# Kernel tuning notes

Hardware: AMD Instinct MI355X
Metric: run time of the kernel (lower is better)

Reference implementation:

```python
import jax, jax.numpy as jnp
import numpy as np

D_MODEL = 1024
SEQ_LEN = 2048
NUM_EIGH = 24
BATCH = 4


def _spectral_filters(L, K):
    # Hankel matrix Z[i,j] = 2 / ((i+j)^3 - (i+j)), 1-indexed; top-K eigvecs scaled by sigma^0.25
    t = np.arange(1, L + 1, dtype=np.float64)
    s = t[:, None] + t[None, :]
    Z = 2.0 / (s ** 3 - s)
    sigma, phi = np.linalg.eigh(Z)
    phi_k = phi[:, -K:] * (sigma[-K:] ** 0.25)
    return jnp.asarray(phi_k, dtype=jnp.float32)


def setup_inputs() -> dict:
    key = jax.random.key(0)
    k1, k2, k3 = jax.random.split(key, 3)
    std = 1.0 / np.sqrt(D_MODEL)
    return {
        "x": jax.random.normal(k1, (BATCH, SEQ_LEN, D_MODEL), dtype=jnp.float32),
        "M_inputs": jax.random.normal(k2, (D_MODEL, D_MODEL), dtype=jnp.float32) * std,
        "M_filters": jax.random.normal(k3, (NUM_EIGH, D_MODEL), dtype=jnp.float32) * std,
        "phi": _spectral_filters(SEQ_LEN, NUM_EIGH),
    }


def _convolve_approx(u, v, n):
    # u: [B, L, D] inputs (already projected); v: [L, D] per-channel causal filters.
    # Dual-branch causal FFT convolution:
    #   plus[b,t,d]  = sum_{s<=t} v[s,d] * u[b,t-s,d]
    #   minus[b,t,d] = (-1)^t * sum_{s<=t} v[s,d] * (-1)^{t-s} u[b,t-s,d]
    B, L, D = u.shape
    sgn = jnp.where(jnp.arange(L) % 2 == 0, 1.0, -1.0).astype(u.dtype)[None, :, None]  # [1,L,1]
    V = jnp.fft.rfft(v, n=n, axis=0)                     # [F, D] complex
    U = jnp.stack([u, u * sgn], axis=-1)                 # [B, L, D, 2]
    Uf = jnp.fft.rfft(U, n=n, axis=1)                    # [B, F, D, 2]
    conv = jnp.fft.irfft(V[None, :, :, None] * Uf, n=n, axis=1)[:, :L]  # [B, L, D, 2]
    return conv[..., 0], conv[..., 1] * sgn


def reference(x, M_inputs, M_filters, phi):
    L = x.shape[1]
    n = 1 << int(np.ceil(np.log2(2 * L - 1)))  # next pow2 of 2L-1 (static)
    x_proj = x @ M_inputs                       # [B, L, D]
    phi_proj = phi[:L] @ M_filters              # [L, D]
    spectral_plus, spectral_minus = _convolve_approx(x_proj, phi_proj, n)
    return spectral_plus + spectral_minus
```

## Files before the change

### kernel.cpp

```cpp
#include <hip/hip_runtime.h>
#include <stdint.h>

#define D_MODEL 1024
#define SEQ 2048
#define HALF 1024
#define K_EIG 24
#define GUARD4 24
#define K4 128
#define K4P (GUARD4 + K4)
#define WE_JP4 72

typedef __attribute__((ext_vector_type(8))) short bf16x8;
typedef __attribute__((ext_vector_type(4))) float f32x4;
typedef _Float16 f16;
typedef _Float16 f16x2 __attribute__((ext_vector_type(2)));
typedef unsigned int uint;

#define GAS __attribute__((address_space(1)))
#define LAS __attribute__((address_space(3)))

static __device__ __forceinline__ unsigned short f2bf(float f) {
  union { float f; uint32_t u; } v; v.f = f;
  uint32_t u = v.u;
  u += 0x7FFFu + ((u >> 16) & 1u);
  return (unsigned short)(u >> 16);
}

static __device__ __forceinline__ float dot2(uint w2, uint u2, float c) {
  return __builtin_amdgcn_fdot2(__builtin_bit_cast(f16x2, w2),
                                __builtin_bit_cast(f16x2, u2), c, false);
}

static __device__ __forceinline__ uint pkrtz(float lo, float hi) {
  return __builtin_bit_cast(uint, __builtin_amdgcn_cvt_pkrtz(lo, hi));
}

__global__ void k_convert_x(const float* __restrict__ x, unsigned short* __restrict__ xb, int n4) {
  int idx = blockIdx.x * blockDim.x + threadIdx.x;
  if (idx < n4) {
    float4 v = ((const float4*)x)[idx];
    ushort4 o;
    o.x = f2bf(v.x); o.y = f2bf(v.y); o.z = f2bf(v.z); o.w = f2bf(v.w);
    ((ushort4*)xb)[idx] = o;
  }
}

__global__ void k_zero_guard(uint4* __restrict__ u4) {
  int idx = blockIdx.x * 256 + threadIdx.x;
  int r = blockIdx.y;
  u4[(size_t)r * (K4P * 1024) + idx] = make_uint4(0u, 0u, 0u, 0u);
}

__global__ void k_transpose_M(const float* __restrict__ M, unsigned short* __restrict__ Mt) {
  __shared__ float tile[32][33];
  int k0 = blockIdx.y * 32, n0 = blockIdx.x * 32;
  int tx = threadIdx.x & 31, ty = threadIdx.x >> 5;
  #pragma unroll
  for (int r = 0; r < 32; r += 8)
    tile[ty + r][tx] = M[(size_t)(k0 + ty + r) * D_MODEL + n0 + tx];
  __syncthreads();
  #pragma unroll
  for (int r = 0; r < 32; r += 8)
    Mt[(size_t)(n0 + ty + r) * D_MODEL + k0 + tx] = f2bf(tile[tx][ty + r]);
}

__global__ __launch_bounds__(256) void k_we4(const float* __restrict__ phi,
                                             const float* __restrict__ Mf,
                                             uint4* __restrict__ we4) {
  const int jp4 = blockIdx.x;
  const int d = blockIdx.y * 256 + threadIdx.x;
  if (jp4 >= 64) {
    we4[(size_t)jp4 * D_MODEL + d] = make_uint4(0u, 0u, 0u, 0u);
    return;
  }
  __shared__ float ph[8][K_EIG];
  if (threadIdx.x < 8 * K_EIG) {
    int s = threadIdx.x / K_EIG, k = threadIdx.x - s * K_EIG;
    ph[s][k] = phi[(size_t)(16 * jp4 + 2 * s) * K_EIG + k];
  }
  __syncthreads();
  float s[8] = {};
  #pragma unroll
  for (int k = 0; k < K_EIG; ++k) {
    float mv = Mf[(size_t)k * D_MODEL + d];
    #pragma unroll
    for (int j = 0; j < 8; ++j) s[j] = fmaf(ph[j][k], mv, s[j]);
  }
  uint4 o;
  o.x = pkrtz(2.f * s[0], 2.f * s[1]);
  o.y = pkrtz(2.f * s[2], 2.f * s[3]);
  o.z = pkrtz(2.f * s[4], 2.f * s[5]);
  o.w = pkrtz(2.f * s[6], 2.f * s[7]);
  we4[(size_t)jp4 * D_MODEL + d] = o;
}

__global__ __launch_bounds__(256) void k_gemm(const unsigned short* __restrict__ A,
                                              const unsigned short* __restrict__ Bt,
                                              uint* __restrict__ Ug) {
  __shared__ unsigned short As[128 * 32];
  __shared__ unsigned short Bs[128 * 32];
  const int m0 = (int)blockIdx.x * 128;
  const int n0 = (int)blockIdx.y * 128;
  const int tid = threadIdx.x;
  const int lane = tid & 63;
  const int wave = tid >> 6;
  const int wm = wave >> 1, wn = wave & 1;
  const int srow = lane >> 2;
  const int skoff = (lane & 3) * 8;

  f32x4 acc[4][4] = {};

  for (int k0 = 0; k0 < 1024; k0 += 32) {
    __syncthreads();
    #pragma unroll
    for (int c = 0; c < 2; ++c) {
      int rbase = wave * 32 + c * 16;
      const unsigned short* src = A + (size_t)(m0 + rbase + srow) * 1024 + k0 + skoff;
      __builtin_amdgcn_global_load_lds((const GAS void*)src, (LAS void*)(As + rbase * 32), 16, 0, 0);
    }
    #pragma unroll
    for (int c = 0; c < 2; ++c) {
      int rbase = wave * 32 + c * 16;
      const unsigned short* src = Bt + (size_t)(n0 + rbase + srow) * 1024 + k0 + skoff;
      __builtin_amdgcn_global_load_lds((const GAS void*)src, (LAS void*)(Bs + rbase * 32), 16, 0, 0);
    }
    __syncthreads();

    bf16x8 a[4], b[4];
    #pragma unroll
    for (int mt = 0; mt < 4; ++mt)
      a[mt] = *(const bf16x8*)(As + ((wm * 64 + mt * 16 + (lane & 15)) * 32 + (lane >> 4) * 8));
    #pragma unroll
    for (int nt = 0; nt < 4; ++nt)
      b[nt] = *(const bf16x8*)(Bs + ((wn * 64 + nt * 16 + (lane & 15)) * 32 + (lane >> 4) * 8));
    #pragma unroll
    for (int mt = 0; mt < 4; ++mt)
      #pragma unroll
      for (int nt = 0; nt < 4; ++nt)
        acc[mt][nt] = __builtin_amdgcn_mfma_f32_16x16x32_bf16(a[mt], b[nt], acc[mt][nt], 0, 0, 0);
  }

  const int crow = (lane >> 4) * 4;
  const int ccol = lane & 15;
  #pragma unroll
  for (int mt = 0; mt < 4; ++mt) {
    int m = m0 + wm * 64 + mt * 16 + crow;
    int b_ = m >> 11;
    int t0 = m & 2047;
    int r_e = b_ << 1;
    int k4 = t0 >> 4;
    int dwo = (t0 >> 2) & 3;
    size_t base_e = ((size_t)(r_e * K4P + GUARD4 + k4) * 1024) * 4 + dwo;
    size_t base_o = ((size_t)((r_e + 1) * K4P + GUARD4 + k4) * 1024) * 4 + dwo;
    #pragma unroll
    for (int nt = 0; nt < 4; ++nt) {
      int n = n0 + wn * 64 + nt * 16 + ccol;
      Ug[base_e + (size_t)n * 4] = pkrtz(acc[mt][nt][0], acc[mt][nt][2]);
      Ug[base_o + (size_t)n * 4] = pkrtz(acc[mt][nt][1], acc[mt][nt][3]);
    }
  }
}

__global__ __launch_bounds__(512, 6) void k_conv(const uint4* __restrict__ u4,
                                                 const uint4* __restrict__ we4,
                                                 float* __restrict__ out) {
  __shared__ uint4 u_r[32 * 64];
  __shared__ uint4 w_s[2][8][64];
  const int flat = blockIdx.x;
  const int dt = flat & 15;
  const int r  = (flat >> 4) & 7;
  const int a  = 7 - (flat >> 7);
  const int d0 = dt * 64;
  const int tid = threadIdx.x;
  const int dl = tid & 63;
  const int ig = tid >> 6;

  const uint4* ub = u4 + ((size_t)r * K4P + GUARD4) * 1024 + d0;
  const int b_ = r >> 1, p = r & 1;

#define STAGEU(k40)                                                                     \
  {                                                                                     \
    int k4e = (k40) + ig;                                                               \
    const uint4* src = ub + (long long)k4e * 1024 + dl;                                 \
    __builtin_amdgcn_global_load_lds((const GAS void*)src,                              \
                                     (LAS void*)(u_r + (k4e & 31) * 64), 16, 0, 0);     \
  }

#define STAGEW(ch)                                                                      \
  {                                                                                     \
    const uint4* src = we4 + (size_t)((ch) * 8 + ig) * 1024 + d0 + dl;                  \
    __builtin_amdgcn_global_load_lds((const GAS void*)src,                              \
                                     (LAS void*)(&w_s[(ch) & 1][ig][0]), 16, 0, 0);     \
  }

  const int i0 = a * 128;
  const int ibase = i0 + ig * 16;
  const int niter = (2 * a + 2) < 8 ? (2 * a + 2) : 8;

  STAGEU(16 * a - 8); STAGEU(16 * a); STAGEU(16 * a + 8);
  STAGEW(0);
  __syncthreads();

  float acc[16];
#pragma unroll
  for (int o = 0; o < 16; ++o) acc[o] = 0.f;

#pragma unroll 1
  for (int c = 0; c < niter; ++c) {
    STAGEU(16 * a - 8 * c - 16);
    STAGEW(c + 1);
    const int cb = c & 1;
    const int kbase = 16 * a + 2 * ig - 8 * c - 2;
#pragma unroll
    for (int s = 0; s < 4; ++s) {
      const int kb = kbase - 2 * s;
      uint4 v0 = u_r[((kb + 0) & 31) * 64 + dl];
      uint4 v1 = u_r[((kb + 1) & 31) * 64 + dl];
      uint4 v2 = u_r[((kb + 2) & 31) * 64 + dl];
      uint4 v3 = u_r[((kb + 3) & 31) * 64 + dl];
      uint P[16];
      P[0] = v0.x; P[1] = v0.y; P[2] = v0.z; P[3] = v0.w;
      P[4] = v1.x; P[5] = v1.y; P[6] = v1.z; P[7] = v1.w;
      P[8] = v2.x; P[9] = v2.y; P[10] = v2.z; P[11] = v2.w;
      P[12] = v3.x; P[13] = v3.y; P[14] = v3.z; P[15] = v3.w;
      uint4 wv0 = w_s[cb][2 * s][dl];
      uint4 wv1 = w_s[cb][2 * s + 1][dl];
      uint W[8];
      W[0] = wv0.x; W[1] = wv0.y; W[2] = wv0.z; W[3] = wv0.w;
      W[4] = wv1.x; W[5] = wv1.y; W[6] = wv1.z; W[7] = wv1.w;
      uint WS[8];
#pragma unroll
      for (int q = 0; q < 8; ++q) WS[q] = __builtin_amdgcn_alignbit(W[q], W[q], 16);
      uint pe[15];
#pragma unroll
      for (int j = 0; j < 15; ++j) pe[j] = __builtin_amdgcn_perm(P[j + 1], P[j], 0x03020504u);
#pragma unroll
      for (int q = 0; q < 8; ++q) {
#pragma unroll
        for (int h = 0; h < 8; ++h) {
          acc[2 * h]     = dot2(W[q],  pe[7 - q + h], acc[2 * h]);
          acc[2 * h + 1] = dot2(WS[q], P[8 - q + h],  acc[2 * h + 1]);
        }
      }
    }
    __syncthreads();
  }

#pragma unroll
  for (int o = 0; o < 16; ++o)
    out[((size_t)b_ * SEQ + 2 * (ibase + o) + p) * D_MODEL + d0 + dl] = acc[o];
#undef STAGEU
#undef STAGEW
}

extern "C" void kernel_launch(void* const* d_in, const int* in_sizes, int n_in,
                              void* d_out, int out_size, void* d_ws, size_t ws_size,
                              hipStream_t stream) {
  const float* x   = (const float*)d_in[0];
  const float* Mi  = (const float*)d_in[1];
  const float* Mf  = (const float*)d_in[2];
  const float* phi = (const float*)d_in[3];
  float* out = (float*)d_out;

  unsigned short* x_bf = (unsigned short*)d_out;
  unsigned short* Mt   = (unsigned short*)((char*)d_out + (16u << 20));

  char* ws = (char*)d_ws;
  uint4* we4 = (uint4*)(ws);
  uint4* u4  = (uint4*)(ws + (2u << 20));

  hipLaunchKernelGGL(k_zero_guard, dim3(96, 8), dim3(256), 0, stream, u4);
  hipLaunchKernelGGL(k_convert_x, dim3(8192), dim3(256), 0, stream, x, x_bf, 2097152);
  hipLaunchKernelGGL(k_transpose_M, dim3(32, 32), dim3(256), 0, stream, Mi, Mt);
  hipLaunchKernelGGL(k_we4, dim3(72, 4), dim3(256), 0, stream, phi, Mf, we4);
  hipLaunchKernelGGL(k_gemm, dim3(64, 8), dim3(256), 0, stream, x_bf, Mt, (uint*)u4);
  hipLaunchKernelGGL(k_conv, dim3(1024), dim3(512), 0, stream, u4, we4, out);
}
```

Measured before the change: 121.2 us.

## Fuse fp32-to-bf16 conversion of x into GEMM A-tile load and swizzle block order

Drops the separate k_convert_x kernel. The GEMM now reads fp32 x directly, converts it to bf16 in registers and writes it to LDS, which removes a full write and re-read of the bf16 copy of x and one launch. It also switches to a 1D grid with a swizzled block-to-tile mapping, so that blocks sharing the same M rows run close together for L2 reuse. In exchange, each GEMM block now reads twice as many bytes of A per tile. It also loses the asynchronous global-to-LDS path for A and does the conversion arithmetic inside the main loop.

Result: slower. 126.5 us (+4.4%).

```diff
diff --git a/kernel.cpp b/kernel.cpp
--- a/kernel.cpp
+++ b/kernel.cpp
@@ -35,14 +35,8 @@
   return __builtin_bit_cast(uint, __builtin_amdgcn_cvt_pkrtz(lo, hi));
 }
 
-__global__ void k_convert_x(const float* __restrict__ x, unsigned short* __restrict__ xb, int n4) {
-  int idx = blockIdx.x * blockDim.x + threadIdx.x;
-  if (idx < n4) {
-    float4 v = ((const float4*)x)[idx];
-    ushort4 o;
-    o.x = f2bf(v.x); o.y = f2bf(v.y); o.z = f2bf(v.z); o.w = f2bf(v.w);
-    ((ushort4*)xb)[idx] = o;
-  }
+static __device__ __forceinline__ uint pkbf(float lo, float hi) {
+  return (uint)f2bf(lo) | ((uint)f2bf(hi) << 16);
 }
 
 __global__ void k_zero_guard(uint4* __restrict__ u4) {
@@ -94,13 +88,15 @@
   we4[(size_t)jp4 * D_MODEL + d] = o;
 }
 
-__global__ __launch_bounds__(256) void k_gemm(const unsigned short* __restrict__ A,
+__global__ __launch_bounds__(256) void k_gemm(const float* __restrict__ X,
                                               const unsigned short* __restrict__ Bt,
                                               uint* __restrict__ Ug) {
   __shared__ unsigned short As[128 * 32];
   __shared__ unsigned short Bs[128 * 32];
-  const int m0 = (int)blockIdx.x * 128;
-  const int n0 = (int)blockIdx.y * 128;
+  const int bid = (int)blockIdx.x;
+  const int swz = (bid & 7) * 64 + (bid >> 3);
+  const int m0 = (swz >> 3) * 128;
+  const int n0 = (swz & 7) * 128;
   const int tid = threadIdx.x;
   const int lane = tid & 63;
   const int wave = tid >> 6;
@@ -108,22 +104,32 @@
   const int srow = lane >> 2;
   const int skoff = (lane & 3) * 8;
 
+  const int arow = tid >> 1;
+  const int akh  = (tid & 1) * 16;
+  const float* xsrc = X + (size_t)(m0 + arow) * 1024 + akh;
+  unsigned short* adst = As + arow * 32 + akh;
+
   f32x4 acc[4][4] = {};
 
   for (int k0 = 0; k0 < 1024; k0 += 32) {
     __syncthreads();
-    #pragma unroll
-    for (int c = 0; c < 2; ++c) {
-      int rbase = wave * 32 + c * 16;
-      const unsigned short* src = A + (size_t)(m0 + rbase + srow) * 1024 + k0 + skoff;
-      __builtin_amdgcn_global_load_lds((const GAS void*)src, (LAS void*)(As + rbase * 32), 16, 0, 0);
-    }
+    float4 xv0 = *(const float4*)(xsrc + k0);
+    float4 xv1 = *(const float4*)(xsrc + k0 + 4);
+    float4 xv2 = *(const float4*)(xsrc + k0 + 8);
+    float4 xv3 = *(const float4*)(xsrc + k0 + 12);
     #pragma unroll
     for (int c = 0; c < 2; ++c) {
       int rbase = wave * 32 + c * 16;
       const unsigned short* src = Bt + (size_t)(n0 + rbase + srow) * 1024 + k0 + skoff;
       __builtin_amdgcn_global_load_lds((const GAS void*)src, (LAS void*)(Bs + rbase * 32), 16, 0, 0);
     }
+    uint4 w0, w1;
+    w0.x = pkbf(xv0.x, xv0.y); w0.y = pkbf(xv0.z, xv0.w);
+    w0.z = pkbf(xv1.x, xv1.y); w0.w = pkbf(xv1.z, xv1.w);
+    w1.x = pkbf(xv2.x, xv2.y); w1.y = pkbf(xv2.z, xv2.w);
+    w1.z = pkbf(xv3.x, xv3.y); w1.w = pkbf(xv3.z, xv3.w);
+    *(uint4*)(adst) = w0;
+    *(uint4*)(adst + 8) = w1;
     __syncthreads();
 
     bf16x8 a[4], b[4];
@@ -262,17 +268,15 @@
   const float* phi = (const float*)d_in[3];
   float* out = (float*)d_out;
 
-  unsigned short* x_bf = (unsigned short*)d_out;
-  unsigned short* Mt   = (unsigned short*)((char*)d_out + (16u << 20));
+  unsigned short* Mt = (unsigned short*)d_out;
 
   char* ws = (char*)d_ws;
   uint4* we4 = (uint4*)(ws);
   uint4* u4  = (uint4*)(ws + (2u << 20));
 
   hipLaunchKernelGGL(k_zero_guard, dim3(96, 8), dim3(256), 0, stream, u4);
-  hipLaunchKernelGGL(k_convert_x, dim3(8192), dim3(256), 0, stream, x, x_bf, 2097152);
   hipLaunchKernelGGL(k_transpose_M, dim3(32, 32), dim3(256), 0, stream, Mi, Mt);
   hipLaunchKernelGGL(k_we4, dim3(72, 4), dim3(256), 0, stream, phi, Mf, we4);
-  hipLaunchKernelGGL(k_gemm, dim3(64, 8), dim3(256), 0, stream, x_bf, Mt, (uint*)u4);
+  hipLaunchKernelGGL(k_gemm, dim3(512), dim3(256), 0, stream, x, Mt, (uint*)u4);
   hipLaunchKernelGGL(k_conv, dim3(1024), dim3(512), 0, stream, u4, we4, out);
 }
```
